# Kernel optimization log

Hardware: AMD Instinct MI355X
Metric: run time of the kernel (lower is better)

Reference implementation:

```python
import jax, jax.numpy as jnp
import numpy as np
import math


def custom_round(x):
    # floor(x - sign(x)*tiny + 0.5): consistent tie-breaking at .5 boundaries
    tiny = jnp.finfo(x.dtype).eps
    return jnp.floor(x - jnp.sign(x) * tiny + 0.5)


def g_x(x):
    # f(x) with the coordinate of largest rounding error pushed to the
    # next-nearest integer (parity-flip candidate). x: [N, d]
    f = custom_round(x)
    delta = jnp.abs(x - f)
    k = jnp.argmax(delta, axis=-1)                      # [N]
    mask = jax.nn.one_hot(k, x.shape[-1], dtype=jnp.bool_)  # [N, d]
    # direction of the flip, matching the original branchy logic:
    #   x>=0: +1 if f < x else -1 ; x<0: +1 if f <= x else -1
    up = jnp.where(x >= 0, f < x, f <= x)
    adj = f + jnp.where(up, 1.0, -1.0).astype(x.dtype)
    return jnp.where(mask, adj, f)


def closest_point_Dn(x):
    f = custom_round(x)
    even = (jnp.mod(jnp.sum(f, axis=-1), 2.0) == 0.0)[:, None]
    return jnp.where(even, f, g_x(x))


def closest_point_E8(x):
    # E8 = D8 union (D8 + 1/2): take the better of the two cosets
    y0 = closest_point_Dn(x)
    y1 = closest_point_Dn(x - 0.5) + 0.5
    d0 = jnp.sum((x - y0) ** 2, axis=-1, keepdims=True)
    d1 = jnp.sum((x - y1) ** 2, axis=-1, keepdims=True)
    return jnp.where(d0 < d1, y0, y1)


def make_tie_dither(d=8):
    irr = np.sqrt(np.array([2, 3, 5, 7, 11, 13, 17, 19][:d], dtype=np.float32))
    u = irr - np.floor(irr) - 0.5
    u = u / np.linalg.norm(u)
    delta = (2.0 ** -40) * 0.5
    return jnp.asarray(delta * u, dtype=jnp.float32)


def setup_inputs() -> dict:
    key = jax.random.key(0)
    kx, _ = jax.random.split(key)
    N, d = 4_000_000, 8
    x = jax.random.normal(kx, (N, d), dtype=jnp.float32) * 2.0
    beta = jnp.array(1.0, dtype=jnp.float32)
    eps = make_tie_dither(d)
    return {"x": x, "beta": beta, "eps": eps}


def reference(x, beta, eps):
    # Lattice quantization with learnable scale and tie dither:
    # y = beta * Q_E8(x / beta + eps)
    z = x / beta + eps[None, :]
    q = closest_point_E8(z)
    return beta * q
```

## Files before the change

kernel.cpp:

```cpp
#include <hip/hip_runtime.h>

#pragma clang fp contract(off)

#define TINY_EPS 1.1920928955078125e-07f

typedef float f4 __attribute__((ext_vector_type(4)));
typedef float f2 __attribute__((ext_vector_type(2)));

__global__ void __launch_bounds__(256)
e8_quant_kernel(const float* __restrict__ x, const float* __restrict__ beta_p,
                const float* __restrict__ eps, float* __restrict__ out, int N) {
    __shared__ float tile[256][12];
    int tid = threadIdx.x;
    int i   = blockIdx.x * 256 + tid;
    bool full_block = ((blockIdx.x + 1) * 256) <= N;
    if (!full_block && i >= N) return;

    float beta = *beta_p;
    bool  b1   = (beta == 1.0f);

    const f4* ep = reinterpret_cast<const f4*>(eps);
    f4 e0 = ep[0], e1 = ep[1];
    float e[8] = {e0.x, e0.y, e0.z, e0.w, e1.x, e1.y, e1.z, e1.w};

    const f4* xp = reinterpret_cast<const f4*>(x) + (size_t)i * 2;
    f4 a = xp[0];
    f4 b = xp[1];
    float z[8] = {a.x, a.y, a.z, a.w, b.x, b.y, b.z, b.w};

    if (b1) {
#pragma unroll
        for (int j = 0; j < 8; ++j) z[j] = z[j] + e[j];
    } else {
#pragma unroll
        for (int j = 0; j < 8; ++j) z[j] = z[j] / beta + e[j];
    }

    f2 fpk[8], dpk[8];
    f2 fsum = {0.0f, 0.0f};
#pragma unroll
    for (int j = 0; j < 8; ++j) {
        f2 xv = {z[j], z[j] - 0.5f};
        f2 cs = {__builtin_copysignf(TINY_EPS, xv.x),
                 __builtin_copysignf(TINY_EPS, xv.y)};
        f2 t  = xv - cs;
        f2 u  = t + 0.5f;
        f2 fv = {floorf(u.x), floorf(u.y)};
        fpk[j] = fv;
        dpk[j] = xv - fv;
        fsum   = fsum + fv;
    }
    bool oddA = (((int)fsum.x) & 1) != 0;
    bool oddB = (((int)fsum.y) & 1) != 0;

    int   kA = 0,        kB = 0;
    float bdA = dpk[0].x, fkA = fpk[0].x;
    float bdB = dpk[0].y, fkB = fpk[0].y;
#pragma unroll
    for (int j = 1; j < 8; ++j) {
        bool bA = fabsf(dpk[j].x) > fabsf(bdA);
        bdA = bA ? dpk[j].x : bdA;
        fkA = bA ? fpk[j].x : fkA;
        kA  = bA ? j : kA;
        bool bB = fabsf(dpk[j].y) > fabsf(bdB);
        bdB = bB ? dpk[j].y : bdB;
        fkB = bB ? fpk[j].y : fkB;
        kB  = bB ? j : kB;
    }
    bool  upA    = (fkA < 0.0f) ? (bdA >= 0.0f) : (bdA > 0.0f);
    float adjA   = fkA + (upA ? 1.0f : -1.0f);
    bool  upB    = (fkB < 0.0f) ? (bdB >= 0.0f) : (bdB > 0.0f);
    float adjB05 = (fkB + (upB ? 1.0f : -1.0f)) + 0.5f;
    int kA2 = oddA ? kA : 8;
    int kB2 = oddB ? kB : 8;

    f2 dacc = {0.0f, 0.0f};
    float yAs[8], yBs[8];
#pragma unroll
    for (int j = 0; j < 8; ++j) {
        bool  mA  = (j == kA2);
        bool  mB  = (j == kB2);
        float yA  = mA ? adjA : fpk[j].x;
        float yBh = fpk[j].y + 0.5f;
        float yB  = mB ? adjB05 : yBh;
        yAs[j] = yA;
        yBs[j] = yB;
        f2 v = {__fsub_rn(z[j], yA),
                __fsub_rn(z[j], yB)};
        dacc = dacc + v * v;
    }
    bool pick0 = dacc.x < dacc.y;

    float q[8];
    if (b1) {
#pragma unroll
        for (int j = 0; j < 8; ++j) q[j] = pick0 ? yAs[j] : yBs[j];
    } else {
#pragma unroll
        for (int j = 0; j < 8; ++j) q[j] = __fmul_rn(beta, pick0 ? yAs[j] : yBs[j]);
    }

    if (full_block) {
        f4* trow = reinterpret_cast<f4*>(&tile[tid][0]);
        f4 w0 = {q[0], q[1], q[2], q[3]};
        f4 w1 = {q[4], q[5], q[6], q[7]};
        trow[0] = w0;
        trow[1] = w1;
        __syncthreads();
        int wave = tid >> 6, lane = tid & 63;
        int wb   = wave << 6;
        f4* op   = reinterpret_cast<f4*>(out) + (size_t)blockIdx.x * 512 + wave * 128;
#pragma unroll
        for (int c = 0; c < 2; ++c) {
            int p = wb + c * 32 + (lane >> 1);
            int h = (lane & 1) << 2;
            f4 v = *reinterpret_cast<const f4*>(&tile[p][h]);
            __builtin_nontemporal_store(v, op + c * 64 + lane);
        }
    } else {
        f4* op = reinterpret_cast<f4*>(out) + (size_t)i * 2;
        f4 s0 = {q[0], q[1], q[2], q[3]};
        f4 s1 = {q[4], q[5], q[6], q[7]};
        op[0] = s0;
        op[1] = s1;
    }
}

extern "C" void kernel_launch(void* const* d_in, const int* in_sizes, int n_in,
                              void* d_out, int out_size, void* d_ws, size_t ws_size,
                              hipStream_t stream) {
    const float* x      = (const float*)d_in[0];
    const float* beta_p = (const float*)d_in[1];
    const float* eps    = (const float*)d_in[2];
    float*       out    = (float*)d_out;

    int N     = in_sizes[0] / 8;
    int block = 256;
    int grid  = (N + block - 1) / block;
    hipLaunchKernelGGL(e8_quant_kernel, dim3(grid), dim3(block), 0, stream,
                       x, beta_p, eps, out, N);
}
```

Before: 41.47 us.

## Convert to grid-stride persistent kernel with register prefetch of next tile

Measured after the change: 46.72 us. +12.6%, slower.

```diff
diff --git a/kernel.cpp b/kernel.cpp
--- a/kernel.cpp
+++ b/kernel.cpp
@@ -7,35 +7,8 @@
 typedef float f4 __attribute__((ext_vector_type(4)));
 typedef float f2 __attribute__((ext_vector_type(2)));
 
-__global__ void __launch_bounds__(256)
-e8_quant_kernel(const float* __restrict__ x, const float* __restrict__ beta_p,
-                const float* __restrict__ eps, float* __restrict__ out, int N) {
-    __shared__ float tile[256][12];
-    int tid = threadIdx.x;
-    int i   = blockIdx.x * 256 + tid;
-    bool full_block = ((blockIdx.x + 1) * 256) <= N;
-    if (!full_block && i >= N) return;
-
-    float beta = *beta_p;
-    bool  b1   = (beta == 1.0f);
-
-    const f4* ep = reinterpret_cast<const f4*>(eps);
-    f4 e0 = ep[0], e1 = ep[1];
-    float e[8] = {e0.x, e0.y, e0.z, e0.w, e1.x, e1.y, e1.z, e1.w};
-
-    const f4* xp = reinterpret_cast<const f4*>(x) + (size_t)i * 2;
-    f4 a = xp[0];
-    f4 b = xp[1];
-    float z[8] = {a.x, a.y, a.z, a.w, b.x, b.y, b.z, b.w};
-
-    if (b1) {
-#pragma unroll
-        for (int j = 0; j < 8; ++j) z[j] = z[j] + e[j];
-    } else {
-#pragma unroll
-        for (int j = 0; j < 8; ++j) z[j] = z[j] / beta + e[j];
-    }
-
+__device__ __forceinline__ void e8_compute(const float z[8], bool b1, float beta,
+                                           float q[8]) {
     f2 fpk[8], dpk[8];
     f2 fsum = {0.0f, 0.0f};
 #pragma unroll
@@ -90,8 +63,6 @@
         dacc = dacc + v * v;
     }
     bool pick0 = dacc.x < dacc.y;
-
-    float q[8];
     if (b1) {
 #pragma unroll
         for (int j = 0; j < 8; ++j) q[j] = pick0 ? yAs[j] : yBs[j];
@@ -99,30 +70,82 @@
 #pragma unroll
         for (int j = 0; j < 8; ++j) q[j] = __fmul_rn(beta, pick0 ? yAs[j] : yBs[j]);
     }
+}
 
-    if (full_block) {
-        f4* trow = reinterpret_cast<f4*>(&tile[tid][0]);
-        f4 w0 = {q[0], q[1], q[2], q[3]};
-        f4 w1 = {q[4], q[5], q[6], q[7]};
-        trow[0] = w0;
-        trow[1] = w1;
-        __syncthreads();
-        int wave = tid >> 6, lane = tid & 63;
-        int wb   = wave << 6;
-        f4* op   = reinterpret_cast<f4*>(out) + (size_t)blockIdx.x * 512 + wave * 128;
+__global__ void __launch_bounds__(256)
+e8_quant_kernel(const float* __restrict__ x, const float* __restrict__ beta_p,
+                const float* __restrict__ eps, float* __restrict__ out,
+                int N, int T ) {
+    __shared__ float tile[256][12];
+    const int tid = threadIdx.x;
+
+    float beta = *beta_p;
+    bool  b1   = (beta == 1.0f);
+    const f4* ep = reinterpret_cast<const f4*>(eps);
+    f4 e0 = ep[0], e1 = ep[1];
+    float e[8] = {e0.x, e0.y, e0.z, e0.w, e1.x, e1.y, e1.z, e1.w};
+
+    const f4* xv = reinterpret_cast<const f4*>(x);
+    f4*       ov = reinterpret_cast<f4*>(out);
+    const int stride = gridDim.x;
+
+    int t = blockIdx.x;
+    int  i0  = t * 256 + tid;
+    int  ic  = (i0 < N) ? i0 : (N - 1);
+    f4 a = xv[(size_t)ic * 2 + 0];
+    f4 b = xv[(size_t)ic * 2 + 1];
+
+    while (t < T) {
+        int tn = t + stride;
+        f4 an = a, bn = b;
+        if (tn < T) {
+            int in = tn * 256 + tid;
+            int inc = (in < N) ? in : (N - 1);
+            an = xv[(size_t)inc * 2 + 0];
+            bn = xv[(size_t)inc * 2 + 1];
+        }
+
+        float z[8] = {a.x, a.y, a.z, a.w, b.x, b.y, b.z, b.w};
+        if (b1) {
 #pragma unroll
-        for (int c = 0; c < 2; ++c) {
-            int p = wb + c * 32 + (lane >> 1);
-            int h = (lane & 1) << 2;
-            f4 v = *reinterpret_cast<const f4*>(&tile[p][h]);
-            __builtin_nontemporal_store(v, op + c * 64 + lane);
+            for (int j = 0; j < 8; ++j) z[j] = z[j] + e[j];
+        } else {
+#pragma unroll
+            for (int j = 0; j < 8; ++j) z[j] = z[j] / beta + e[j];
         }
-    } else {
-        f4* op = reinterpret_cast<f4*>(out) + (size_t)i * 2;
-        f4 s0 = {q[0], q[1], q[2], q[3]};
-        f4 s1 = {q[4], q[5], q[6], q[7]};
-        op[0] = s0;
-        op[1] = s1;
+        float q[8];
+        e8_compute(z, b1, beta, q);
+
+        bool full = (t * 256 + 256) <= N;
+        if (full) {
+            f4* trow = reinterpret_cast<f4*>(&tile[tid][0]);
+            f4 w0 = {q[0], q[1], q[2], q[3]};
+            f4 w1 = {q[4], q[5], q[6], q[7]};
+            trow[0] = w0;
+            trow[1] = w1;
+            int wave = tid >> 6, lane = tid & 63;
+            int wb   = wave << 6;
+            f4* op   = ov + (size_t)t * 512 + wave * 128;
+#pragma unroll
+            for (int c = 0; c < 2; ++c) {
+                int p = wb + c * 32 + (lane >> 1);
+                int h = (lane & 1) << 2;
+                f4 v = *reinterpret_cast<const f4*>(&tile[p][h]);
+                __builtin_nontemporal_store(v, op + c * 64 + lane);
+            }
+        } else {
+            int i = t * 256 + tid;
+            if (i < N) {
+                f4 s0 = {q[0], q[1], q[2], q[3]};
+                f4 s1 = {q[4], q[5], q[6], q[7]};
+                ov[(size_t)i * 2 + 0] = s0;
+                ov[(size_t)i * 2 + 1] = s1;
+            }
+        }
+
+        t = tn;
+        a = an;
+        b = bn;
     }
 }
 
@@ -134,9 +157,9 @@
     const float* eps    = (const float*)d_in[2];
     float*       out    = (float*)d_out;
 
-    int N     = in_sizes[0] / 8;
-    int block = 256;
-    int grid  = (N + block - 1) / block;
-    hipLaunchKernelGGL(e8_quant_kernel, dim3(grid), dim3(block), 0, stream,
-                       x, beta_p, eps, out, N);
+    int N = in_sizes[0] / 8;
+    int T = (N + 255) / 256;
+    int grid = T < 2048 ? T : 2048;
+    hipLaunchKernelGGL(e8_quant_kernel, dim3(grid), dim3(256), 0, stream,
+                       x, beta_p, eps, out, N, T);
 }
```
